# Kernel tuning notes

Hardware: AMD Instinct MI355X
Metric: run time of the kernel (lower is better)

## Reference

```python
import jax, jax.numpy as jnp
import numpy as np

N_HEAD = 16
D_HEAD = 64  # d_model=1024 // n_head=16


def setup_inputs() -> dict:
    key = jax.random.key(0)
    ks = jax.random.split(key, 8)
    B, S, D = 2, 2048, 1024
    scale = 1.0 / np.sqrt(D)
    return {
        "q": jax.random.normal(ks[0], (B, S, D), jnp.float32),
        "k": jax.random.normal(ks[1], (B, S, D), jnp.float32),
        "v": jax.random.normal(ks[2], (B, S, D), jnp.float32),
        "w_q": jax.random.normal(ks[3], (D, D), jnp.float32) * scale,
        "w_k": jax.random.normal(ks[4], (D, D), jnp.float32) * scale,
        "w_v": jax.random.normal(ks[5], (D, D), jnp.float32) * scale,
        "w_fc": jax.random.normal(ks[6], (D, D), jnp.float32) * scale,
        "b_fc": jnp.zeros((D,), jnp.float32),
    }


def reference(q, k, v, w_q, w_k, w_v, w_fc, b_fc):
    B, Sq, D = q.shape
    # projections (torch Linear: x @ W.T), split into heads -> [B, H, S, Dh]
    def proj(x, w):
        return (x @ w.T).reshape(B, x.shape[1], N_HEAD, D_HEAD).transpose(0, 2, 1, 3)
    qh, kh, vh = proj(q, w_q), proj(k, w_k), proj(v, w_v)
    # scaled dot-product attention with explicit weights (dropout = identity, eval mode)
    scores = jnp.einsum("bhqd,bhkd->bhqk", qh, kh) / jnp.sqrt(jnp.float32(D_HEAD))
    attn = jax.nn.softmax(scores, axis=-1)  # [B, H, Sq, Sk]
    ctx = jnp.einsum("bhqk,bhkd->bhqd", attn, vh)
    ctx = ctx.transpose(0, 2, 1, 3).reshape(B, Sq, D)
    out = ctx @ w_fc.T + b_fc
    return out, attn
```

## Files before the change

kernel.cpp:

```cpp
#include <hip/hip_runtime.h>


using f16   = _Float16;
using f16x4 = __attribute__((ext_vector_type(4))) f16;
using f16x8 = __attribute__((ext_vector_type(8))) f16;
using f32x4 = __attribute__((ext_vector_type(4))) float;

#define MFMA16(a, b, c) __builtin_amdgcn_mfma_f32_16x16x32_f16((a), (b), (c), 0, 0, 0)

__device__ static inline float fexp2(float x) {
#if __has_builtin(__builtin_amdgcn_exp2f)
  return __builtin_amdgcn_exp2f(x);
#else
  return exp2f(x);
#endif
}

#define C1 0.18033688011112042f

#define WB(IMM)                                                        \
  do {                                                                 \
    asm volatile("s_waitcnt vmcnt(" #IMM ") lgkmcnt(0)" ::: "memory"); \
    __builtin_amdgcn_s_barrier();                                      \
  } while (0)

__device__ static inline void gld16(const void* gptr, void* lptr) {
  __builtin_amdgcn_global_load_lds(
      (const __attribute__((address_space(1))) void*)gptr,
      (__attribute__((address_space(3))) void*)lptr, 16, 0, 0);
}

__device__ static inline unsigned int pack2(float a, float b) {
  union { f16 h[2]; unsigned int u; } x;
  x.h[0] = (f16)a; x.h[1] = (f16)b;
  return x.u;
}

__global__ __launch_bounds__(256) void cast_all(
    const float* __restrict__ q, const float* __restrict__ k,
    const float* __restrict__ v, const float* __restrict__ wq,
    const float* __restrict__ wk, const float* __restrict__ wv,
    const float* __restrict__ wfc, f16* __restrict__ ws) {
  int i = blockIdx.x * 256 + threadIdx.x;
  const float* src;
  f16* dst;
  int li;
  if (i < 3145728) {
    if (i < 1048576)      { src = q; dst = ws;            li = i; }
    else if (i < 2097152) { src = k; dst = ws + 4194304;  li = i - 1048576; }
    else                  { src = v; dst = ws + 8388608;  li = i - 2097152; }
  } else {
    int j = i - 3145728;
    int wsel = j >> 18;
    src = (wsel == 0) ? wq : (wsel == 1) ? wk : (wsel == 2) ? wv : wfc;
    dst = ws + 12582912 + wsel * 1048576;
    li = j & 262143;
  }
  float4 x = ((const float4*)src)[li];
  f16x4 y;
  y[0] = (f16)x.x; y[1] = (f16)x.y; y[2] = (f16)x.z; y[3] = (f16)x.w;
  ((f16x4*)dst)[li] = y;
}

template <int MODE, int BN>
__global__ __launch_bounds__(256) void gemm_bt(
    const f16* __restrict__ A0, const f16* __restrict__ W0,
    const float* __restrict__ bias, void* __restrict__ Cout) {
  constexpr int FJ = BN / 32;
  __shared__ unsigned short XA[8192];
  __shared__ unsigned short WB2[BN * 64];
  int tid = threadIdx.x;
  int w = tid >> 6, l = tid & 63, lq = l & 15, g = l >> 4;
  int nb3 = blockIdx.x * BN, mb = blockIdx.y * 128;
  int wsel = (MODE == 4) ? (nb3 >> 10) : 0;
  int nb = (MODE == 4) ? (nb3 & 1023) : nb3;
  const f16* A = (MODE == 4) ? A0 + (size_t)wsel * 4194304 : A0;
  const f16* W = (MODE == 4) ? W0 + (size_t)wsel * 1048576 : W0;
  bool swapR = (MODE == 4) && (wsel == 2);
  int wi = w >> 1, wj = w & 1;

  f32x4 acc[4][FJ];
#pragma unroll
  for (int i = 0; i < 4; i++)
#pragma unroll
    for (int j = 0; j < FJ; j++) acc[i][j] = (f32x4){0.f, 0.f, 0.f, 0.f};

  char* Xb = (char*)XA;
  char* Wb = (char*)WB2;
  int row = tid >> 3;
  int c = (tid & 7) ^ (row & 7);
  const f16* Asrc = A + (size_t)(mb + row) * 1024 + c * 8;
  const f16* Wsrc = W + (size_t)(nb + row) * 1024 + c * 8;

  for (int k0 = 0; k0 < 1024; k0 += 64) {
#pragma unroll
    for (int i2 = 0; i2 < 4; i2++)
      gld16(Asrc + k0 + i2 * 32 * 1024, Xb + i2 * 4096 + w * 1024);
#pragma unroll
    for (int i2 = 0; i2 < BN / 32; i2++)
      gld16(Wsrc + k0 + i2 * 32 * 1024, Wb + i2 * 4096 + w * 1024);
    __syncthreads();

    const char* at = swapR ? Wb : Xb;
    const char* bt = swapR ? Xb : Wb;

    f16x8 bfr[FJ][2];
#pragma unroll
    for (int f = 0; f < FJ; f++) {
      int r = wj * (BN / 2) + f * 16 + lq;
      int sw = (r & 7) << 4;
      bfr[f][0] = *(const f16x8*)(bt + r * 128 + ((g * 16) ^ sw));
      bfr[f][1] = *(const f16x8*)(bt + r * 128 + ((64 + g * 16) ^ sw));
    }
#pragma unroll
    for (int fi = 0; fi < 4; fi++) {
      int r = wi * 64 + fi * 16 + lq;
      int sw = (r & 7) << 4;
      f16x8 a0 = *(const f16x8*)(at + r * 128 + ((g * 16) ^ sw));
      f16x8 a1 = *(const f16x8*)(at + r * 128 + ((64 + g * 16) ^ sw));
#pragma unroll
      for (int fj = 0; fj < FJ; fj++) {
        acc[fi][fj] = MFMA16(a0, bfr[fj][0], acc[fi][fj]);
        acc[fi][fj] = MFMA16(a1, bfr[fj][1], acc[fi][fj]);
      }
    }
    __syncthreads();
  }

#pragma unroll
  for (int fi = 0; fi < 4; fi++) {
#pragma unroll
    for (int fj = 0; fj < FJ; fj++) {
#pragma unroll
      for (int jj = 0; jj < 4; jj++) {
        float v = acc[fi][fj][jj];
        int iG = (swapR ? nb : mb) + wi * 64 + fi * 16 + g * 4 + jj;
        int jG = (swapR ? mb : nb) + wj * (BN / 2) + fj * 16 + lq;
        if constexpr (MODE == 3) {
          int m2 = iG, n2 = jG;
          ((float*)Cout)[(size_t)m2 * 1024 + n2] = v + bias[n2];
        } else {
          f16* dstb = (f16*)Cout + (size_t)wsel * 4194304;
          if (!swapR) {
            int m2 = iG, n2 = jG;
            size_t dst = (size_t)((m2 >> 11) * 16 + (n2 >> 6)) * 131072 +
                         (size_t)(m2 & 2047) * 64 + (n2 & 63);
            dstb[dst] = (f16)v;
          } else {
            int n2 = iG, m2 = jG;
            size_t dst = (size_t)((m2 >> 11) * 1024 + n2) * 2048 + (m2 & 2047);
            dstb[dst] = (f16)v;
          }
        }
      }
    }
  }
}

__global__ __launch_bounds__(256, 2) void attn_fused(
    const f16* __restrict__ qh, const f16* __restrict__ kh,
    const f16* __restrict__ vt, float* __restrict__ attn,
    f16* __restrict__ ctx) {
  __shared__ unsigned short Kl[4][4096];
  __shared__ unsigned short Vl[4][4096];
  __shared__ unsigned short Pl[8192];
  int tid = threadIdx.x;
  int w = tid >> 6, l = tid & 63, lq = l & 15, g = l >> 4;

  int bid = blockIdx.x;
  int xcd = bid & 7, j = bid >> 3;
  int bh = xcd * 4 + (j >> 4);
  int qt = j & 15;

  const f16* qbase = qh + (size_t)(bh * 2048 + qt * 128 + w * 32 + lq) * 64;
  f16x8 qf[2][2];
#pragma unroll
  for (int f = 0; f < 2; f++) {
    qf[f][0] = *(const f16x8*)(qbase + f * 16 * 64 + g * 8);
    qf[f][1] = *(const f16x8*)(qbase + f * 16 * 64 + 32 + g * 8);
  }
  asm volatile("s_waitcnt vmcnt(0)" ::: "memory");

  char* Kb = (char*)Kl;
  char* Vb = (char*)Vl;
  char* Pw = (char*)Pl + w * 4096;

  int row = tid >> 3;
  int c = (tid & 7) ^ (row & 7);
  const f16* ksrc = kh + (size_t)bh * 131072 + (size_t)row * 64 + c * 8;
  const f16* vsrc = vt + (size_t)bh * 131072 + (size_t)row * 2048 + c * 8;

  int swq = (lq & 7) << 4;

#define KISSUE(i)                                                   \
  do {                                                              \
    const f16* kp_ = ksrc + (size_t)(i) * 4096;                     \
    char* kb_ = Kb + ((i) & 3) * 8192;                              \
    gld16(kp_, kb_ + w * 1024);                                     \
    gld16(kp_ + 2048, kb_ + 4096 + w * 1024);                       \
  } while (0)
#define VISSUE(i)                                                   \
  do {                                                              \
    const f16* vp_ = vsrc + (size_t)(i) * 64;                       \
    char* vb_ = Vb + ((i) & 3) * 8192;                              \
    gld16(vp_, vb_ + w * 1024);                                     \
    gld16(vp_ + 32 * 2048, vb_ + 4096 + w * 1024);                  \
  } while (0)

  float ls[2] = {0.f, 0.f};
  KISSUE(0); KISSUE(1); KISSUE(2);
  WB(4);
  for (int t = 0; t < 32; t++) {
    if (t + 3 < 32) KISSUE(t + 3);
    const char* KbC = Kb + (t & 3) * 8192;
#pragma unroll
    for (int cf = 0; cf < 4; cf++) {
      int kr = cf * 16 + lq;
      int sw = (kr & 7) << 4;
      f16x8 ka  = *(const f16x8*)(KbC + kr * 128 + ((g * 16) ^ sw));
      f16x8 kb2 = *(const f16x8*)(KbC + kr * 128 + ((64 + g * 16) ^ sw));
#pragma unroll
      for (int f = 0; f < 2; f++) {
        f32x4 s = (f32x4){0.f, 0.f, 0.f, 0.f};
        s = MFMA16(ka, qf[f][0], s);
        s = MFMA16(kb2, qf[f][1], s);
        ls[f] += fexp2(s[0] * C1) + fexp2(s[1] * C1) +
                 fexp2(s[2] * C1) + fexp2(s[3] * C1);
      }
    }
    if (t < 29) { WB(4); } else { WB(0); }
  }
  float linv[2];
#pragma unroll
  for (int f = 0; f < 2; f++) {
    float t2 = ls[f];
    t2 += __shfl_xor(t2, 16);
    t2 += __shfl_xor(t2, 32);
    linv[f] = 1.0f / t2;
  }

  f32x4 acc[2][4];
#pragma unroll
  for (int f = 0; f < 2; f++)
#pragma unroll
    for (int i = 0; i < 4; i++) acc[f][i] = (f32x4){0.f, 0.f, 0.f, 0.f};

  float* attnrow0 =
      attn + ((size_t)bh * 2048 + qt * 128 + w * 32 + lq) * 2048;
  float* attnrow1 = attnrow0 + 16 * 2048;

  KISSUE(0); VISSUE(0); KISSUE(1); VISSUE(1); KISSUE(2); VISSUE(2);
  WB(8);
  for (int t = 0; t < 32; t++) {
    int kt = t * 64;
    if (t + 3 < 32) { KISSUE(t + 3); VISSUE(t + 3); }
    const char* KbC = Kb + (t & 3) * 8192;
    const char* VbC = Vb + (t & 3) * 8192;

#pragma unroll
    for (int cf = 0; cf < 4; cf++) {
      int kr = cf * 16 + lq;
      int sw = (kr & 7) << 4;
      f16x8 ka  = *(const f16x8*)(KbC + kr * 128 + ((g * 16) ^ sw));
      f16x8 kb2 = *(const f16x8*)(KbC + kr * 128 + ((64 + g * 16) ^ sw));
      int k0 = cf * 16 + g * 4;
#pragma unroll
      for (int f = 0; f < 2; f++) {
        f32x4 s = (f32x4){0.f, 0.f, 0.f, 0.f};
        s = MFMA16(ka, qf[f][0], s);
        s = MFMA16(kb2, qf[f][1], s);
        float e0 = fexp2(s[0] * C1) * linv[f];
        float e1 = fexp2(s[1] * C1) * linv[f];
        float e2 = fexp2(s[2] * C1) * linv[f];
        float e3 = fexp2(s[3] * C1) * linv[f];
        float4 o = {e0, e1, e2, e3};
        *(float4*)((f ? attnrow1 : attnrow0) + kt + cf * 16 + g * 4) = o;
        char* Pr = Pw + (f * 16 + lq) * 128;
        *(unsigned int*)(Pr + ((k0 * 2) ^ swq))       = pack2(e0, e1);
        *(unsigned int*)(Pr + (((k0 + 2) * 2) ^ swq)) = pack2(e2, e3);
      }
    }

    {
      f16x8 pb[2][2];
#pragma unroll
      for (int f = 0; f < 2; f++) {
        char* Pr = Pw + (f * 16 + lq) * 128;
        pb[f][0] = *(const f16x8*)(Pr + ((g * 16) ^ swq));
        pb[f][1] = *(const f16x8*)(Pr + ((64 + g * 16) ^ swq));
      }
#pragma unroll
      for (int af = 0; af < 4; af++) {
        int vr = af * 16 + lq;
        int sv = (vr & 7) << 4;
        f16x8 va0 = *(const f16x8*)(VbC + vr * 128 + ((g * 16) ^ sv));
        f16x8 va1 = *(const f16x8*)(VbC + vr * 128 + ((64 + g * 16) ^ sv));
#pragma unroll
        for (int f = 0; f < 2; f++) {
          acc[f][af] = MFMA16(va0, pb[f][0], acc[f][af]);
          acc[f][af] = MFMA16(va1, pb[f][1], acc[f][af]);
        }
      }
    }
    if (t == 0)       { WB(16); }
    else if (t == 1)  { WB(24); }
    else if (t == 2)  { WB(28); }
    else if (t == 29) { WB(28); }
    else if (t == 30) { WB(24); }
    else if (t == 31) { WB(8);  }
    else              { WB(32); }
  }

#pragma unroll
  for (int f = 0; f < 2; f++) {
    char* Pr = Pw + (f * 16 + lq) * 128;
#pragma unroll
    for (int af = 0; af < 4; af++) {
#pragma unroll
      for (int jj = 0; jj < 4; jj += 2) {
        int dh0 = af * 16 + g * 4 + jj;
        *(unsigned int*)(Pr + ((dh0 * 2) ^ swq)) =
            pack2(acc[f][af][jj], acc[f][af][jj + 1]);
      }
    }
  }
  {
    int q2 = l >> 1, cc = l & 1;
    int swr = (q2 & 7) << 4;
    int b = bh >> 4, h = bh & 15;
    f16* crow =
        ctx + ((size_t)b * 2048 + qt * 128 + w * 32 + q2) * 1024 + h * 64;
#pragma unroll
    for (int t2 = 0; t2 < 4; t2++) {
      f16x8 v2 = *(const f16x8*)(Pw + q2 * 128 + ((cc * 64 + t2 * 16) ^ swr));
      *(f16x8*)(crow + cc * 32 + t2 * 8) = v2;
    }
  }
#undef KISSUE
#undef VISSUE
}

extern "C" void kernel_launch(void* const* d_in, const int* in_sizes, int n_in,
                              void* d_out, int out_size, void* d_ws,
                              size_t ws_size, hipStream_t stream) {
  (void)in_sizes; (void)n_in; (void)out_size; (void)ws_size;
  const float* q   = (const float*)d_in[0];
  const float* k   = (const float*)d_in[1];
  const float* v   = (const float*)d_in[2];
  const float* wq  = (const float*)d_in[3];
  const float* wk  = (const float*)d_in[4];
  const float* wv  = (const float*)d_in[5];
  const float* wfc = (const float*)d_in[6];
  const float* bfc = (const float*)d_in[7];

  f16* ws = (f16*)d_ws;
  f16* qf   = ws;
  f16* wqf  = ws + 12582912;
  f16* wfcf = ws + 15728640;
  f16* qhp  = ws + 16777216;
  f16* khp  = ws + 20971520;
  f16* vtp  = ws + 25165824;
  f16* ctxp = ws + 29360128;

  float* outp  = (float*)d_out;
  float* attnp = outp + 4194304;

  cast_all<<<16384, 256, 0, stream>>>(q, k, v, wq, wk, wv, wfc, ws);
  gemm_bt<4, 128><<<dim3(24, 32), 256, 0, stream>>>(qf, wqf, nullptr, qhp);
  attn_fused<<<512, 256, 0, stream>>>(qhp, khp, vtp, attnp, ctxp);
  gemm_bt<3, 64><<<dim3(16, 32), 256, 0, stream>>>(ctxp, wfcf, bfc, outp);
}
```

Measured before the change: 295.3 us.

## Stage attention probabilities in LDS for coalesced row-wise attn stores

Instead of each lane writing scattered float4 fragments of the attention matrix every tile, the fp16 P tiles for two consecutive K tiles are kept in a doubled per-wave LDS buffer. Every other iteration they are read back row by row and written as contiguous 512-byte float rows. The K/V ring drops from four buffers to three (two in the first pass) with retuned vmcnt waits, to make room for the larger P buffer. The goal is more efficient writes of the very large attn output, but attn values are now rounded through fp16 before being written, and prefetch depth is reduced.

Measured after the change: 274.9 us. 1.07x faster.

```diff
diff --git a/kernel.cpp b/kernel.cpp
--- a/kernel.cpp
+++ b/kernel.cpp
@@ -18,7 +18,7 @@
 
 #define C1 0.18033688011112042f
 
-#define WB(IMM)                                                        \
+#define WAIT_BARRIER(IMM)                                              \
   do {                                                                 \
     asm volatile("s_waitcnt vmcnt(" #IMM ") lgkmcnt(0)" ::: "memory"); \
     __builtin_amdgcn_s_barrier();                                      \
@@ -161,9 +161,9 @@
     const f16* __restrict__ qh, const f16* __restrict__ kh,
     const f16* __restrict__ vt, float* __restrict__ attn,
     f16* __restrict__ ctx) {
-  __shared__ unsigned short Kl[4][4096];
-  __shared__ unsigned short Vl[4][4096];
-  __shared__ unsigned short Pl[8192];
+  __shared__ unsigned short Kl[3][4096];
+  __shared__ unsigned short Vl[3][4096];
+  __shared__ unsigned short Pl[16384];
   int tid = threadIdx.x;
   int w = tid >> 6, l = tid & 63, lq = l & 15, g = l >> 4;
 
@@ -183,7 +183,7 @@
 
   char* Kb = (char*)Kl;
   char* Vb = (char*)Vl;
-  char* Pw = (char*)Pl + w * 4096;
+  char* Pw = (char*)Pl + w * 8192;
 
   int row = tid >> 3;
   int c = (tid & 7) ^ (row & 7);
@@ -192,27 +192,27 @@
 
   int swq = (lq & 7) << 4;
 
-#define KISSUE(i)                                                   \
+#define KISSUE(i, b_)                                               \
   do {                                                              \
     const f16* kp_ = ksrc + (size_t)(i) * 4096;                     \
-    char* kb_ = Kb + ((i) & 3) * 8192;                              \
+    char* kb_ = Kb + (b_) * 8192;                                   \
     gld16(kp_, kb_ + w * 1024);                                     \
     gld16(kp_ + 2048, kb_ + 4096 + w * 1024);                       \
   } while (0)
-#define VISSUE(i)                                                   \
+#define VISSUE(i, b_)                                               \
   do {                                                              \
     const f16* vp_ = vsrc + (size_t)(i) * 64;                       \
-    char* vb_ = Vb + ((i) & 3) * 8192;                              \
+    char* vb_ = Vb + (b_) * 8192;                                   \
     gld16(vp_, vb_ + w * 1024);                                     \
     gld16(vp_ + 32 * 2048, vb_ + 4096 + w * 1024);                  \
   } while (0)
 
   float ls[2] = {0.f, 0.f};
-  KISSUE(0); KISSUE(1); KISSUE(2);
-  WB(4);
+  KISSUE(0, 0);
+  WAIT_BARRIER(0);
   for (int t = 0; t < 32; t++) {
-    if (t + 3 < 32) KISSUE(t + 3);
-    const char* KbC = Kb + (t & 3) * 8192;
+    if (t < 31) KISSUE(t + 1, (t + 1) & 1);
+    const char* KbC = Kb + (t & 1) * 8192;
 #pragma unroll
     for (int cf = 0; cf < 4; cf++) {
       int kr = cf * 16 + lq;
@@ -228,7 +228,7 @@
                  fexp2(s[2] * C1) + fexp2(s[3] * C1);
       }
     }
-    if (t < 29) { WB(4); } else { WB(0); }
+    WAIT_BARRIER(0);
   }
   float linv[2];
 #pragma unroll
@@ -245,17 +245,25 @@
 #pragma unroll
     for (int i = 0; i < 4; i++) acc[f][i] = (f32x4){0.f, 0.f, 0.f, 0.f};
 
-  float* attnrow0 =
-      attn + ((size_t)bh * 2048 + qt * 128 + w * 32 + lq) * 2048;
-  float* attnrow1 = attnrow0 + 16 * 2048;
-
-  KISSUE(0); VISSUE(0); KISSUE(1); VISSUE(1); KISSUE(2); VISSUE(2);
-  WB(8);
+  float* attnw =
+      attn + ((size_t)bh * 2048 + qt * 128 + w * 32) * 2048;
+
+  int rsub = l >> 5;
+  int c4 = (l & 31) * 4;
+  int sb = c4 * 2;
+  int shalf = sb & 128;
+  int slocal = sb & 127;
+
+  KISSUE(0, 0); VISSUE(0, 0);
+  KISSUE(1, 1); VISSUE(1, 1);
+  WAIT_BARRIER(4);
+  int bc = 0;
   for (int t = 0; t < 32; t++) {
-    int kt = t * 64;
-    if (t + 3 < 32) { KISSUE(t + 3); VISSUE(t + 3); }
-    const char* KbC = Kb + (t & 3) * 8192;
-    const char* VbC = Vb + (t & 3) * 8192;
+    int bn = bc + 2; if (bn >= 3) bn -= 3;
+    if (t + 2 < 32) { KISSUE(t + 2, bn); VISSUE(t + 2, bn); }
+    const char* KbC = Kb + bc * 8192;
+    const char* VbC = Vb + bc * 8192;
+    int hb = (t & 1) * 128;
 
 #pragma unroll
     for (int cf = 0; cf < 4; cf++) {
@@ -273,9 +281,7 @@
         float e1 = fexp2(s[1] * C1) * linv[f];
         float e2 = fexp2(s[2] * C1) * linv[f];
         float e3 = fexp2(s[3] * C1) * linv[f];
-        float4 o = {e0, e1, e2, e3};
-        *(float4*)((f ? attnrow1 : attnrow0) + kt + cf * 16 + g * 4) = o;
-        char* Pr = Pw + (f * 16 + lq) * 128;
+        char* Pr = Pw + (f * 16 + lq) * 256 + hb;
         *(unsigned int*)(Pr + ((k0 * 2) ^ swq))       = pack2(e0, e1);
         *(unsigned int*)(Pr + (((k0 + 2) * 2) ^ swq)) = pack2(e2, e3);
       }
@@ -285,7 +291,7 @@
       f16x8 pb[2][2];
 #pragma unroll
       for (int f = 0; f < 2; f++) {
-        char* Pr = Pw + (f * 16 + lq) * 128;
+        char* Pr = Pw + (f * 16 + lq) * 256 + hb;
         pb[f][0] = *(const f16x8*)(Pr + ((g * 16) ^ swq));
         pb[f][1] = *(const f16x8*)(Pr + ((64 + g * 16) ^ swq));
       }
@@ -302,18 +308,28 @@
         }
       }
     }
-    if (t == 0)       { WB(16); }
-    else if (t == 1)  { WB(24); }
-    else if (t == 2)  { WB(28); }
-    else if (t == 29) { WB(28); }
-    else if (t == 30) { WB(24); }
-    else if (t == 31) { WB(8);  }
-    else              { WB(32); }
+
+    if (t & 1) {
+      float* abase = attnw + (t - 1) * 64 + c4;
+#pragma unroll
+      for (int i = 0; i < 16; i++) {
+        int r = i * 2 + rsub;
+        f16x4 pv = *(const f16x4*)(Pw + r * 256 + shalf +
+                                   (slocal ^ ((r & 7) << 4)));
+        float4 o = {(float)pv[0], (float)pv[1], (float)pv[2], (float)pv[3]};
+        *(float4*)(abase + (size_t)r * 2048) = o;
+      }
+    }
+
+    if (t == 0)      { WAIT_BARRIER(4);  }
+    else if (t >= 30){ WAIT_BARRIER(16); }
+    else             { WAIT_BARRIER(20); }
+    bc = (bc == 2) ? 0 : bc + 1;
   }
 
 #pragma unroll
   for (int f = 0; f < 2; f++) {
-    char* Pr = Pw + (f * 16 + lq) * 128;
+    char* Pr = Pw + (f * 16 + lq) * 256;
 #pragma unroll
     for (int af = 0; af < 4; af++) {
 #pragma unroll
@@ -332,7 +348,7 @@
         ctx + ((size_t)b * 2048 + qt * 128 + w * 32 + q2) * 1024 + h * 64;
 #pragma unroll
     for (int t2 = 0; t2 < 4; t2++) {
-      f16x8 v2 = *(const f16x8*)(Pw + q2 * 128 + ((cc * 64 + t2 * 16) ^ swr));
+      f16x8 v2 = *(const f16x8*)(Pw + q2 * 256 + ((cc * 64 + t2 * 16) ^ swr));
       *(f16x8*)(crow + cc * 32 + t2 * 8) = v2;
     }
   }
```
